# Optimization experiments

Measured on AMD Instinct MI355X. Metric: run time of the kernel, lower is better.

Reference implementation:

```python
import jax, jax.numpy as jnp
import numpy as np

N_NODES = 524288
N_EDGES = 4194304
NUM_GRAPHS = 4096
F_IN = 4
PHI_HID = 128
PHI_OUT = 128
F_HID = 256
SCORE_DIM = 2


def _glorot(key, fan_in, fan_out):
    s = jnp.sqrt(2.0 / (fan_in + fan_out)).astype(jnp.float32)
    return jax.random.normal(key, (fan_in, fan_out), dtype=jnp.float32) * s


def setup_inputs() -> dict:
    key = jax.random.key(0)
    ks = jax.random.split(key, 16)
    x = jax.random.normal(ks[0], (N_NODES, F_IN), dtype=jnp.float32)
    edge_index = jax.random.randint(ks[1], (2, N_EDGES), 0, N_NODES, dtype=jnp.int64)
    batch = jnp.sort(jax.random.randint(ks[2], (N_NODES,), 0, NUM_GRAPHS, dtype=jnp.int64))
    # Phi MLP: in -> hid -> hid -> out (num_layers=2 hidden blocks)
    phi_w0 = _glorot(ks[3], F_IN, PHI_HID); phi_b0 = jnp.zeros((PHI_HID,), jnp.float32)
    phi_w1 = _glorot(ks[4], PHI_HID, PHI_HID); phi_b1 = jnp.zeros((PHI_HID,), jnp.float32)
    phi_w2 = _glorot(ks[5], PHI_HID, PHI_OUT); phi_b2 = jnp.zeros((PHI_OUT,), jnp.float32)
    # F MLP head: in -> hid -> hid -> score_dim
    f_w0 = _glorot(ks[6], PHI_OUT, F_HID); f_b0 = jnp.zeros((F_HID,), jnp.float32)
    f_w1 = _glorot(ks[7], F_HID, F_HID); f_b1 = jnp.zeros((F_HID,), jnp.float32)
    f_w2 = _glorot(ks[8], F_HID, SCORE_DIM); f_b2 = jnp.zeros((SCORE_DIM,), jnp.float32)
    return {"x": x, "edge_index": edge_index, "batch": batch,
            "phi_w0": phi_w0, "phi_b0": phi_b0, "phi_w1": phi_w1, "phi_b1": phi_b1,
            "phi_w2": phi_w2, "phi_b2": phi_b2,
            "f_w0": f_w0, "f_b0": f_b0, "f_w1": f_w1, "f_b1": f_b1,
            "f_w2": f_w2, "f_b2": f_b2}


def reference(x, edge_index, batch,
              phi_w0, phi_b0, phi_w1, phi_b1, phi_w2, phi_b2,
              f_w0, f_b0, f_w1, f_b1, f_w2, f_b2):
    # PhiMessagePassing.update ignores aggr_out: the scatter-add over edge_index
    # is mathematically dead. Node update = phi(x) per node.
    h = jax.nn.relu(x @ phi_w0 + phi_b0)          # [N, PHI_HID]
    h = jax.nn.relu(h @ phi_w1 + phi_b1)          # [N, PHI_HID]
    h = h @ phi_w2 + phi_b2                        # [N, PHI_OUT]
    # global_add_pool: segment sum by graph id
    g = jax.ops.segment_sum(h, batch, num_segments=NUM_GRAPHS)  # [G, PHI_OUT]
    # F head MLP
    g = jax.nn.relu(g @ f_w0 + f_b0)
    g = jax.nn.relu(g @ f_w1 + f_b1)
    out = g @ f_w2 + f_b2                          # [G, SCORE_DIM]
    return out
```

## Files before the change

### kernel.cpp

```cpp
#include <hip/hip_runtime.h>
#include <hip/hip_bf16.h>

#define NNODES   524288
#define NGRAPHS  4096
#define HG       4
#define GS       12

typedef __attribute__((ext_vector_type(8)))  short short8;
typedef __attribute__((ext_vector_type(4)))  float f32x4;
typedef __attribute__((ext_vector_type(16))) float f32x16;

static __device__ __forceinline__ unsigned short f2bf(float f) {
    __hip_bfloat16 h = __float2bfloat16(f);
    return *reinterpret_cast<unsigned short*>(&h);
}

static __device__ __forceinline__ int swz(int node, int chunk) {
    return node * 128 + ((chunk ^ (node & 15)) << 3);
}

__global__ __launch_bounds__(256) void prep_weights(
        const float* __restrict__ w0, const float* __restrict__ b0,
        const float* __restrict__ w1,
        const float* __restrict__ w2, const float* __restrict__ fw0,
        const float* __restrict__ b2,
        unsigned short* __restrict__ w0F, unsigned short* __restrict__ w1F,
        float* __restrict__ W0p, float* __restrict__ c0p,
        float* __restrict__ Pz) {
    const int e = blockIdx.x * 256 + threadIdx.x;
    if (e < 132096)
        reinterpret_cast<float4*>(Pz)[e] = make_float4(0.f, 0.f, 0.f, 0.f);
    if (e < 16384) {
        const int j = e & 7, lane = (e >> 3) & 63, ks = (e >> 9) & 7, q = (e >> 12) & 3;
        const int of = q * 32 + (lane & 31);
        const int k  = ks * 16 + (lane >> 5) * 8 + j;
        w1F[e] = f2bf(w1[k * 128 + of]);
    } else if (e < 18432) {
        const int i = e - 16384;
        const int j = i & 7, lane = (i >> 3) & 63, q = (i >> 9) & 3;
        const int of = q * 32 + (lane & 31);
        const int k  = (lane >> 5) * 8 + j;
        unsigned short v = 0;
        if (k < 4)       v = f2bf(w0[k * 128 + of]);
        else if (k == 4) v = f2bf(b0[of]);
        w0F[i] = v;
    } else if (e < 51200) {
        const int i = e - 18432;
        const int o = i & 255, kp = i >> 8;
        float v = 0.f;
        for (int of0 = 0; of0 < 128; of0 += 16) {
            float wa[16], wb[16];
            #pragma unroll
            for (int u = 0; u < 16; ++u) {
                wa[u] = w2[kp * 128 + of0 + u];
                wb[u] = fw0[(of0 + u) * 256 + o];
            }
            #pragma unroll
            for (int u = 0; u < 16; ++u)
                v = fmaf(wa[u], wb[u], v);
        }
        W0p[kp * 256 + o] = v;
    } else if (e < 51456) {
        const int o = e - 51200;
        float v = 0.f;
        #pragma unroll 8
        for (int of = 0; of < 128; ++of)
            v = fmaf(b2[of], fw0[of * 256 + o], v);
        c0p[o] = v;
    }
}

__global__ __launch_bounds__(256, 6) void phi_kernel(
        const float* __restrict__ x, const int* __restrict__ batch,
        const unsigned short* __restrict__ w0F,
        const unsigned short* __restrict__ w1F, const float* __restrict__ b1,
        float* __restrict__ P, float* __restrict__ cnts) {
    __shared__ __align__(16) unsigned short h1[64 * 128];
    const int tid  = threadIdx.x;
    const int lane = tid & 63;
    const int q    = tid >> 6;
    const int n0   = blockIdx.x * 64;
    const int l31  = lane & 31;
    const int h    = lane >> 5;

    const int gi = batch[n0 + lane];
    const int gp = __shfl_up(gi, 1);
    const unsigned long long mask = __ballot((lane == 0) || (gi != gp));

    f32x16 acc[2];

    {
        const short8 af = *reinterpret_cast<const short8*>(w0F + (q*64 + lane)*8);
        short8 bf[2];
        #pragma unroll
        for (int nt = 0; nt < 2; ++nt) {
            const float4 xv = *reinterpret_cast<const float4*>(
                x + (size_t)(n0 + nt*32 + l31) * 4);
            short8 v = (short8){0,0,0,0,0,0,0,0};
            if (h == 0) {
                v[0] = (short)f2bf(xv.x); v[1] = (short)f2bf(xv.y);
                v[2] = (short)f2bf(xv.z); v[3] = (short)f2bf(xv.w);
                v[4] = (short)0x3F80;
            }
            bf[nt] = v;
        }
        acc[0] = (f32x16){}; acc[1] = (f32x16){};
        #pragma unroll
        for (int nt = 0; nt < 2; ++nt)
            acc[nt] = __builtin_amdgcn_mfma_f32_32x32x16_bf16(
                af, bf[nt], acc[nt], 0, 0, 0);
    }
    #pragma unroll
    for (int g4 = 0; g4 < 4; ++g4) {
        #pragma unroll
        for (int nt = 0; nt < 2; ++nt) {
            const int node = nt*32 + l31;
            const f32x16 A = acc[nt];
            ushort4 s;
            s.x = f2bf(fmaxf(A[g4*4+0], 0.f));
            s.y = f2bf(fmaxf(A[g4*4+1], 0.f));
            s.z = f2bf(fmaxf(A[g4*4+2], 0.f));
            s.w = f2bf(fmaxf(A[g4*4+3], 0.f));
            *reinterpret_cast<ushort4*>(&h1[swz(node, q*4 + g4) + h*4]) = s;
        }
    }
    __syncthreads();

    acc[0] = (f32x16){}; acc[1] = (f32x16){};
    #pragma unroll
    for (int ks = 0; ks < 8; ++ks) {
        short8 a[2];
        #pragma unroll
        for (int mtn = 0; mtn < 2; ++mtn)
            a[mtn] = *reinterpret_cast<const short8*>(
                &h1[swz(mtn*32 + l31, ks*2 + h)]);
        const short8 bb = *reinterpret_cast<const short8*>(
            w1F + ((q*8 + ks)*64 + lane)*8);
        #pragma unroll
        for (int mtn = 0; mtn < 2; ++mtn)
            acc[mtn] = __builtin_amdgcn_mfma_f32_32x32x16_bf16(
                a[mtn], bb, acc[mtn], 0, 0, 0);
    }

    const float b1v = b1[q*32 + l31];
    #pragma unroll
    for (int mtn = 0; mtn < 2; ++mtn)
        #pragma unroll
        for (int r = 0; r < 16; ++r)
            acc[mtn][r] = fmaxf(acc[mtn][r] + b1v, 0.f);

    float tot = 0.f;
    #pragma unroll
    for (int mtn = 0; mtn < 2; ++mtn) {
        const f32x16 A = acc[mtn];
        #pragma unroll
        for (int r = 0; r < 16; ++r) tot += A[r];
    }

    if (mask == 1ull) {
        float val = tot + __shfl_xor(tot, 32);
        if (h == 0)
            atomicAdd(P + (size_t)gi * 128 + q*32 + l31, val);
        if (tid == 0)
            atomicAdd(cnts + gi, 64.f);
    } else {
        unsigned long long rem = mask & (mask - 1);
        float below = 0.f;
        int s = 0;
        while (true) {
            const int e = rem ? (int)__builtin_ctzll(rem) : 64;
            const int grun = __shfl(gi, s);
            float run;
            if (e == 64) {
                run = tot - below;
            } else {
                float pref = 0.f;
                #pragma unroll
                for (int mtn = 0; mtn < 2; ++mtn) {
                    const f32x16 A = acc[mtn];
                    #pragma unroll
                    for (int r = 0; r < 16; ++r) {
                        const int node = mtn*32 + (r & 3) + 8*(r >> 2) + 4*h;
                        const float inc = (node < e) ? 1.f : 0.f;
                        pref = fmaf(A[r], inc, pref);
                    }
                }
                run = pref - below;
                below = pref;
            }
            const float val = run + __shfl_xor(run, 32);
            if (h == 0)
                atomicAdd(P + (size_t)grun * 128 + q*32 + l31, val);
            if (tid == 0)
                atomicAdd(cnts + grun, (float)(e - s));
            if (!rem) break;
            s = e;
            rem &= rem - 1;
        }
    }
}

__global__ __launch_bounds__(256, 4) void head_kernel(
        const float* __restrict__ P, const float* __restrict__ cnts,
        const float* __restrict__ W0p, const float* __restrict__ c0p,
        const float* __restrict__ fb0,
        const float* __restrict__ fw1, const float* __restrict__ fb1,
        const float* __restrict__ fw2, const float* __restrict__ fb2,
        float* __restrict__ out) {
    __shared__ float gS[128 * GS];
    __shared__ float h1T[256 * GS];
    __shared__ float red[4][8];
    __shared__ float cntS[HG];
    const int tid = threadIdx.x;
    const int g0  = blockIdx.x * HG;

    if (tid < HG) cntS[tid] = cnts[g0 + tid];
    {
        const int gr = tid >> 6, k0 = (tid & 63) * 2;
        const float2 v = *reinterpret_cast<const float2*>(
            P + (size_t)(g0 + gr) * 128 + k0);
        gS[(k0+0)*GS + gr] = v.x;
        gS[(k0+1)*GS + gr] = v.y;
    }
    __syncthreads();

    float a1[HG];
    #pragma unroll
    for (int i = 0; i < HG; ++i) a1[i] = 0.f;
    for (int k0 = 0; k0 < 128; k0 += 16) {
        float w[16];
        #pragma unroll
        for (int u = 0; u < 16; ++u)
            w[u] = W0p[(k0 + u) * 256 + tid];
        #pragma unroll
        for (int u = 0; u < 16; ++u) {
            const f32x4 v0 = *reinterpret_cast<const f32x4*>(&gS[(k0+u)*GS]);
            #pragma unroll
            for (int j = 0; j < 4; ++j)
                a1[j] = fmaf(v0[j], w[u], a1[j]);
        }
    }
    {
        const float bb = fb0[tid];
        const float cc = c0p[tid];
        f32x4 s0;
        #pragma unroll
        for (int j = 0; j < 4; ++j)
            s0[j] = fmaxf(fmaf(cntS[j], cc, a1[j]) + bb, 0.f);
        *reinterpret_cast<f32x4*>(&h1T[tid*GS]) = s0;
    }
    __syncthreads();

    float a2[HG];
    #pragma unroll
    for (int i = 0; i < HG; ++i) a2[i] = 0.f;
    for (int k0 = 0; k0 < 256; k0 += 16) {
        float w[16];
        #pragma unroll
        for (int u = 0; u < 16; ++u)
            w[u] = fw1[(k0 + u) * 256 + tid];
        #pragma unroll
        for (int u = 0; u < 16; ++u) {
            const f32x4 v0 = *reinterpret_cast<const f32x4*>(&h1T[(k0+u)*GS]);
            #pragma unroll
            for (int j = 0; j < 4; ++j)
                a2[j] = fmaf(v0[j], w[u], a2[j]);
        }
    }

    float p[8];
    {
        const float bb  = fb1[tid];
        const float w2a = fw2[tid*2 + 0];
        const float w2b = fw2[tid*2 + 1];
        #pragma unroll
        for (int i = 0; i < HG; ++i) {
            const float h2 = fmaxf(a2[i] + bb, 0.f);
            p[i*2 + 0] = h2 * w2a;
            p[i*2 + 1] = h2 * w2b;
        }
    }
    #pragma unroll
    for (int i = 0; i < 8; ++i) {
        float v = p[i];
        v += __shfl_xor(v, 32); v += __shfl_xor(v, 16); v += __shfl_xor(v, 8);
        v += __shfl_xor(v, 4);  v += __shfl_xor(v, 2);  v += __shfl_xor(v, 1);
        p[i] = v;
    }
    if ((tid & 63) == 0) {
        #pragma unroll
        for (int i = 0; i < 8; ++i) red[tid >> 6][i] = p[i];
    }
    __syncthreads();
    if (tid < 8)
        out[g0*2 + tid] = red[0][tid] + red[1][tid] + red[2][tid] + red[3][tid]
                        + fb2[tid & 1];
}

extern "C" void kernel_launch(void* const* d_in, const int* in_sizes, int n_in,
                              void* d_out, int out_size, void* d_ws, size_t ws_size,
                              hipStream_t stream) {
    const float* x   = (const float*)d_in[0];
    const int*   batch = (const int*)d_in[2];
    const float* w0  = (const float*)d_in[3];
    const float* b0  = (const float*)d_in[4];
    const float* w1  = (const float*)d_in[5];
    const float* b1  = (const float*)d_in[6];
    const float* w2  = (const float*)d_in[7];
    const float* b2  = (const float*)d_in[8];
    const float* fw0 = (const float*)d_in[9];
    const float* fb0 = (const float*)d_in[10];
    const float* fw1 = (const float*)d_in[11];
    const float* fb1 = (const float*)d_in[12];
    const float* fw2 = (const float*)d_in[13];
    const float* fb2 = (const float*)d_in[14];
    float* out = (float*)d_out;

    float* P    = (float*)d_ws;
    float* cnts = P + (size_t)NGRAPHS * 128;
    unsigned short* w1F = (unsigned short*)(cnts + NGRAPHS);
    unsigned short* w0F = w1F + 16384;
    float* W0p = (float*)(w0F + 2048);
    float* c0p = W0p + 128 * 256;

    prep_weights<<<516, 256, 0, stream>>>(w0, b0, w1, w2, fw0, b2,
                                          w0F, w1F, W0p, c0p, P);
    phi_kernel<<<NNODES / 64, 256, 0, stream>>>(x, batch, w0F, w1F, b1, P, cnts);
    head_kernel<<<NGRAPHS / HG, 256, 0, stream>>>(P, cnts, W0p, c0p, fb0,
                                                  fw1, fb1, fw2, fb2, out);
}
```

Baseline: 153.1 us.

## Fuse prep, phi and head into one cooperative persistent kernel with grid syncs

Merges the weight-prep, per-node phi and per-graph head kernels into a single cooperative kernel launched with a fixed grid of 1024 blocks. Grid-wide syncs replace the boundaries between the three phases, and blocks loop over phi tiles and head chunks persistently. The aim is to remove the launch gaps and tail effects between the three launches. In exchange, the phi stage runs under a stricter launch bound (4 blocks per CU instead of 6) with combined register pressure, and pays for two grid barriers. If the cooperative launch fails, it falls back to the original three-kernel path.

```diff
diff --git a/kernel.cpp b/kernel.cpp
--- a/kernel.cpp
+++ b/kernel.cpp
@@ -1,10 +1,14 @@
 #include <hip/hip_runtime.h>
 #include <hip/hip_bf16.h>
+#include <hip/hip_cooperative_groups.h>
+
+namespace cg = cooperative_groups;
 
 #define NNODES   524288
 #define NGRAPHS  4096
 #define HG       4
 #define GS       12
+#define FGRID    1024
 
 typedef __attribute__((ext_vector_type(8)))  short short8;
 typedef __attribute__((ext_vector_type(4)))  float f32x4;
@@ -19,7 +23,9 @@
     return node * 128 + ((chunk ^ (node & 15)) << 3);
 }
 
-__global__ __launch_bounds__(256) void prep_weights(
+
+static __device__ __forceinline__ void prep_body(
+        int e,
         const float* __restrict__ w0, const float* __restrict__ b0,
         const float* __restrict__ w1,
         const float* __restrict__ w2, const float* __restrict__ fw0,
@@ -27,7 +33,6 @@
         unsigned short* __restrict__ w0F, unsigned short* __restrict__ w1F,
         float* __restrict__ W0p, float* __restrict__ c0p,
         float* __restrict__ Pz) {
-    const int e = blockIdx.x * 256 + threadIdx.x;
     if (e < 132096)
         reinterpret_cast<float4*>(Pz)[e] = make_float4(0.f, 0.f, 0.f, 0.f);
     if (e < 16384) {
@@ -70,16 +75,14 @@
     }
 }
 
-__global__ __launch_bounds__(256, 6) void phi_kernel(
+static __device__ __forceinline__ void phi_tile(
+        int n0, int tid, unsigned short* __restrict__ h1,
         const float* __restrict__ x, const int* __restrict__ batch,
         const unsigned short* __restrict__ w0F,
         const unsigned short* __restrict__ w1F, const float* __restrict__ b1,
         float* __restrict__ P, float* __restrict__ cnts) {
-    __shared__ __align__(16) unsigned short h1[64 * 128];
-    const int tid  = threadIdx.x;
     const int lane = tid & 63;
     const int q    = tid >> 6;
-    const int n0   = blockIdx.x * 64;
     const int l31  = lane & 31;
     const int h    = lane >> 5;
 
@@ -200,6 +203,164 @@
     }
 }
 
+static __device__ __forceinline__ void head_chunk(
+        int g0, int tid, float* __restrict__ smemF,
+        const float* __restrict__ P, const float* __restrict__ cnts,
+        const float* __restrict__ W0p, const float* __restrict__ c0p,
+        const float* __restrict__ fb0,
+        const float* __restrict__ fw1, const float* __restrict__ fb1,
+        const float* __restrict__ fw2, const float* __restrict__ fb2,
+        float* __restrict__ out) {
+    float* gS   = smemF;
+    float* h1T  = gS + 128 * GS;
+    float* red  = h1T + 256 * GS;
+    float* cntS = red + 32;
+
+    if (tid < HG) cntS[tid] = cnts[g0 + tid];
+    {
+        const int gr = tid >> 6, k0 = (tid & 63) * 2;
+        const float2 v = *reinterpret_cast<const float2*>(
+            P + (size_t)(g0 + gr) * 128 + k0);
+        gS[(k0+0)*GS + gr] = v.x;
+        gS[(k0+1)*GS + gr] = v.y;
+    }
+    __syncthreads();
+
+    float a1[HG];
+    #pragma unroll
+    for (int i = 0; i < HG; ++i) a1[i] = 0.f;
+    for (int k0 = 0; k0 < 128; k0 += 16) {
+        float w[16];
+        #pragma unroll
+        for (int u = 0; u < 16; ++u)
+            w[u] = W0p[(k0 + u) * 256 + tid];
+        #pragma unroll
+        for (int u = 0; u < 16; ++u) {
+            const f32x4 v0 = *reinterpret_cast<const f32x4*>(&gS[(k0+u)*GS]);
+            #pragma unroll
+            for (int j = 0; j < 4; ++j)
+                a1[j] = fmaf(v0[j], w[u], a1[j]);
+        }
+    }
+    {
+        const float bb = fb0[tid];
+        const float cc = c0p[tid];
+        f32x4 s0;
+        #pragma unroll
+        for (int j = 0; j < 4; ++j)
+            s0[j] = fmaxf(fmaf(cntS[j], cc, a1[j]) + bb, 0.f);
+        *reinterpret_cast<f32x4*>(&h1T[tid*GS]) = s0;
+    }
+    __syncthreads();
+
+    float a2[HG];
+    #pragma unroll
+    for (int i = 0; i < HG; ++i) a2[i] = 0.f;
+    for (int k0 = 0; k0 < 256; k0 += 16) {
+        float w[16];
+        #pragma unroll
+        for (int u = 0; u < 16; ++u)
+            w[u] = fw1[(k0 + u) * 256 + tid];
+        #pragma unroll
+        for (int u = 0; u < 16; ++u) {
+            const f32x4 v0 = *reinterpret_cast<const f32x4*>(&h1T[(k0+u)*GS]);
+            #pragma unroll
+            for (int j = 0; j < 4; ++j)
+                a2[j] = fmaf(v0[j], w[u], a2[j]);
+        }
+    }
+
+    float p[2*HG];
+    {
+        const float bb  = fb1[tid];
+        const float w2a = fw2[tid*2 + 0];
+        const float w2b = fw2[tid*2 + 1];
+        #pragma unroll
+        for (int i = 0; i < HG; ++i) {
+            const float h2 = fmaxf(a2[i] + bb, 0.f);
+            p[i*2 + 0] = h2 * w2a;
+            p[i*2 + 1] = h2 * w2b;
+        }
+    }
+    #pragma unroll
+    for (int i = 0; i < 2*HG; ++i) {
+        float v = p[i];
+        v += __shfl_xor(v, 32); v += __shfl_xor(v, 16); v += __shfl_xor(v, 8);
+        v += __shfl_xor(v, 4);  v += __shfl_xor(v, 2);  v += __shfl_xor(v, 1);
+        p[i] = v;
+    }
+    if ((tid & 63) == 0) {
+        #pragma unroll
+        for (int i = 0; i < 2*HG; ++i) red[(tid >> 6) * 8 + i] = p[i];
+    }
+    __syncthreads();
+    if (tid < 2*HG)
+        out[g0*2 + tid] = red[0*8 + tid] + red[1*8 + tid] + red[2*8 + tid]
+                        + red[3*8 + tid] + fb2[tid & 1];
+}
+
+
+__global__ __launch_bounds__(256, 4) void fused_kernel(
+        const float* __restrict__ x, const int* __restrict__ batch,
+        const float* __restrict__ w0, const float* __restrict__ b0,
+        const float* __restrict__ w1, const float* __restrict__ b1,
+        const float* __restrict__ w2, const float* __restrict__ fw0,
+        const float* __restrict__ b2, const float* __restrict__ fb0,
+        const float* __restrict__ fw1, const float* __restrict__ fb1,
+        const float* __restrict__ fw2, const float* __restrict__ fb2,
+        float* __restrict__ out,
+        unsigned short* __restrict__ w0F, unsigned short* __restrict__ w1F,
+        float* __restrict__ W0p, float* __restrict__ c0p,
+        float* __restrict__ P, float* __restrict__ cnts) {
+    __shared__ __align__(16) unsigned char smem[18688];
+    const int tid = threadIdx.x;
+    cg::grid_group grid = cg::this_grid();
+
+    prep_body(blockIdx.x * 256 + tid, w0, b0, w1, w2, fw0, b2,
+              w0F, w1F, W0p, c0p, P);
+
+    grid.sync();
+
+    {
+        unsigned short* h1 = reinterpret_cast<unsigned short*>(smem);
+        for (int tile = blockIdx.x; tile < NNODES / 64; tile += gridDim.x) {
+            phi_tile(tile * 64, tid, h1, x, batch, w0F, w1F, b1, P, cnts);
+            __syncthreads();
+        }
+    }
+
+    grid.sync();
+
+    {
+        float* smemF = reinterpret_cast<float*>(smem);
+        for (int hb = blockIdx.x; hb < NGRAPHS / HG; hb += gridDim.x)
+            head_chunk(hb * HG, tid, smemF, P, cnts, W0p, c0p, fb0,
+                       fw1, fb1, fw2, fb2, out);
+    }
+}
+
+
+__global__ __launch_bounds__(256) void prep_weights(
+        const float* __restrict__ w0, const float* __restrict__ b0,
+        const float* __restrict__ w1,
+        const float* __restrict__ w2, const float* __restrict__ fw0,
+        const float* __restrict__ b2,
+        unsigned short* __restrict__ w0F, unsigned short* __restrict__ w1F,
+        float* __restrict__ W0p, float* __restrict__ c0p,
+        float* __restrict__ Pz) {
+    prep_body(blockIdx.x * 256 + threadIdx.x, w0, b0, w1, w2, fw0, b2,
+              w0F, w1F, W0p, c0p, Pz);
+}
+
+__global__ __launch_bounds__(256, 6) void phi_kernel(
+        const float* __restrict__ x, const int* __restrict__ batch,
+        const unsigned short* __restrict__ w0F,
+        const unsigned short* __restrict__ w1F, const float* __restrict__ b1,
+        float* __restrict__ P, float* __restrict__ cnts) {
+    __shared__ __align__(16) unsigned short h1[64 * 128];
+    phi_tile(blockIdx.x * 64, threadIdx.x, h1, x, batch, w0F, w1F, b1, P, cnts);
+}
+
 __global__ __launch_bounds__(256, 4) void head_kernel(
         const float* __restrict__ P, const float* __restrict__ cnts,
         const float* __restrict__ W0p, const float* __restrict__ c0p,
@@ -207,95 +368,11 @@
         const float* __restrict__ fw1, const float* __restrict__ fb1,
         const float* __restrict__ fw2, const float* __restrict__ fb2,
         float* __restrict__ out) {
-    __shared__ float gS[128 * GS];
-    __shared__ float h1T[256 * GS];
-    __shared__ float red[4][8];
-    __shared__ float cntS[HG];
-    const int tid = threadIdx.x;
-    const int g0  = blockIdx.x * HG;
-
-    if (tid < HG) cntS[tid] = cnts[g0 + tid];
-    {
-        const int gr = tid >> 6, k0 = (tid & 63) * 2;
-        const float2 v = *reinterpret_cast<const float2*>(
-            P + (size_t)(g0 + gr) * 128 + k0);
-        gS[(k0+0)*GS + gr] = v.x;
-        gS[(k0+1)*GS + gr] = v.y;
-    }
-    __syncthreads();
-
-    float a1[HG];
-    #pragma unroll
-    for (int i = 0; i < HG; ++i) a1[i] = 0.f;
-    for (int k0 = 0; k0 < 128; k0 += 16) {
-        float w[16];
-        #pragma unroll
-        for (int u = 0; u < 16; ++u)
-            w[u] = W0p[(k0 + u) * 256 + tid];
-        #pragma unroll
-        for (int u = 0; u < 16; ++u) {
-            const f32x4 v0 = *reinterpret_cast<const f32x4*>(&gS[(k0+u)*GS]);
-            #pragma unroll
-            for (int j = 0; j < 4; ++j)
-                a1[j] = fmaf(v0[j], w[u], a1[j]);
-        }
-    }
-    {
-        const float bb = fb0[tid];
-        const float cc = c0p[tid];
-        f32x4 s0;
-        #pragma unroll
-        for (int j = 0; j < 4; ++j)
-            s0[j] = fmaxf(fmaf(cntS[j], cc, a1[j]) + bb, 0.f);
-        *reinterpret_cast<f32x4*>(&h1T[tid*GS]) = s0;
-    }
-    __syncthreads();
-
-    float a2[HG];
-    #pragma unroll
-    for (int i = 0; i < HG; ++i) a2[i] = 0.f;
-    for (int k0 = 0; k0 < 256; k0 += 16) {
-        float w[16];
-        #pragma unroll
-        for (int u = 0; u < 16; ++u)
-            w[u] = fw1[(k0 + u) * 256 + tid];
-        #pragma unroll
-        for (int u = 0; u < 16; ++u) {
-            const f32x4 v0 = *reinterpret_cast<const f32x4*>(&h1T[(k0+u)*GS]);
-            #pragma unroll
-            for (int j = 0; j < 4; ++j)
-                a2[j] = fmaf(v0[j], w[u], a2[j]);
-        }
-    }
-
-    float p[8];
-    {
-        const float bb  = fb1[tid];
-        const float w2a = fw2[tid*2 + 0];
-        const float w2b = fw2[tid*2 + 1];
-        #pragma unroll
-        for (int i = 0; i < HG; ++i) {
-            const float h2 = fmaxf(a2[i] + bb, 0.f);
-            p[i*2 + 0] = h2 * w2a;
-            p[i*2 + 1] = h2 * w2b;
-        }
-    }
-    #pragma unroll
-    for (int i = 0; i < 8; ++i) {
-        float v = p[i];
-        v += __shfl_xor(v, 32); v += __shfl_xor(v, 16); v += __shfl_xor(v, 8);
-        v += __shfl_xor(v, 4);  v += __shfl_xor(v, 2);  v += __shfl_xor(v, 1);
-        p[i] = v;
-    }
-    if ((tid & 63) == 0) {
-        #pragma unroll
-        for (int i = 0; i < 8; ++i) red[tid >> 6][i] = p[i];
-    }
-    __syncthreads();
-    if (tid < 8)
-        out[g0*2 + tid] = red[0][tid] + red[1][tid] + red[2][tid] + red[3][tid]
-                        + fb2[tid & 1];
-}
+    __shared__ __align__(16) float smemF[4644];
+    head_chunk(blockIdx.x * HG, threadIdx.x, smemF, P, cnts, W0p, c0p, fb0,
+               fw1, fb1, fw2, fb2, out);
+}
+
 
 extern "C" void kernel_launch(void* const* d_in, const int* in_sizes, int n_in,
                               void* d_out, int out_size, void* d_ws, size_t ws_size,
@@ -323,9 +400,24 @@
     float* W0p = (float*)(w0F + 2048);
     float* c0p = W0p + 128 * 256;
 
-    prep_weights<<<516, 256, 0, stream>>>(w0, b0, w1, w2, fw0, b2,
-                                          w0F, w1F, W0p, c0p, P);
-    phi_kernel<<<NNODES / 64, 256, 0, stream>>>(x, batch, w0F, w1F, b1, P, cnts);
-    head_kernel<<<NGRAPHS / HG, 256, 0, stream>>>(P, cnts, W0p, c0p, fb0,
-                                                  fw1, fb1, fw2, fb2, out);
-}
+    void* args[] = {
+        (void*)&x, (void*)&batch,
+        (void*)&w0, (void*)&b0, (void*)&w1, (void*)&b1, (void*)&w2,
+        (void*)&fw0, (void*)&b2, (void*)&fb0, (void*)&fw1, (void*)&fb1,
+        (void*)&fw2, (void*)&fb2, (void*)&out,
+        (void*)&w0F, (void*)&w1F, (void*)&W0p, (void*)&c0p,
+        (void*)&P, (void*)&cnts
+    };
+    hipError_t err = hipLaunchCooperativeKernel(
+        reinterpret_cast<const void*>(fused_kernel),
+        dim3(FGRID), dim3(256), args, 0, stream);
+
+    if (err != hipSuccess) {
+        prep_weights<<<516, 256, 0, stream>>>(w0, b0, w1, w2, fw0, b2,
+                                              w0F, w1F, W0p, c0p, P);
+        phi_kernel<<<NNODES / 64, 256, 0, stream>>>(x, batch, w0F, w1F, b1,
+                                                    P, cnts);
+        head_kernel<<<NGRAPHS / HG, 256, 0, stream>>>(P, cnts, W0p, c0p, fb0,
+                                                      fw1, fb1, fw2, fb2, out);
+    }
+}
```

Result: slower. 569.5 us (+271.9%).
